# Performance work log

Hardware: AMD Instinct MI355X
Metric: run time of the kernel (lower is better)

Reference implementation:

```python
import jax, jax.numpy as jnp
import numpy as np

B = 128
DIM = 1024


def setup_inputs() -> dict:
    key = jax.random.key(0)
    k1, k2 = jax.random.split(key)
    return {
        "input1": jax.random.normal(k1, (B, DIM), dtype=jnp.float32),
        "input2": jax.random.normal(k2, (B, DIM), dtype=jnp.float32),
    }


def reference(input1, input2):
    # Original torch module computes, via a dim x dim x dim permutation tensor:
    #   cc[b, i] = sum_t input1[b, (i - t) % dim] * input2[b, t]   (circular convolution)
    # then sums over the batch and reshapes to [1, 1, dim].
    dim = input1.shape[1]
    # idx[i, t] = (i - t) mod dim  -> circulant gather of input1
    idx = (jnp.arange(dim)[:, None] - jnp.arange(dim)[None, :]) % dim
    gathered = input1[:, idx]                      # [B, dim, dim]
    cc = jnp.einsum('bit,bt->bi', gathered, input2)  # per-batch circular conv [B, dim]
    sum_rep = jnp.sum(cc, axis=0)                  # [dim]
    return sum_rep[None, None, :]                  # [1, 1, dim]
```

## Files before the change

kernel.cpp:

```cpp
#include <hip/hip_runtime.h>


#define CC_D 1024

__device__ __forceinline__ int swz(int f) {
  return (f & ~7) | ((f + (f >> 3)) & 7);
}

__global__ __launch_bounds__(512, 8) void cc_partial_kernel(
    const float* __restrict__ X, const float* __restrict__ Y,
    float* __restrict__ ws) {
  const int blk    = blockIdx.x;
  const int b      = blk >> 3;
  const int tslice = blk & 7;
  const int tid    = threadIdx.x;
  const int ig     = tid & 127;
  const int ts     = tid >> 7;

  __shared__ __align__(16) float smem[4096 + 128];
  float4* sm4 = (float4*)smem;
  float*  ysh = smem + 4096;

  if (tid < 256) {
    const float4 v = ((const float4*)(X + b * CC_D))[tid];
    sm4[swz(tid)]       = v;
    sm4[swz(tid + 256)] = v;
  }
  if (tid < 32) {
    ((float4*)ysh)[tid] =
        ((const float4*)(Y + b * CC_D + tslice * 128))[tid];
  }
  __syncthreads();

  const int ts_u = __builtin_amdgcn_readfirstlane(ts);
  const int t0   = tslice * 128 + ts_u * 32;

  const int f0 = 254 + 2 * ig - (t0 >> 2);

  float W[16];
#pragma unroll
  for (int m = 0; m < 4; ++m) {
    const float4 w = sm4[swz(f0 + m)];
    W[4 * m + 0] = w.x; W[4 * m + 1] = w.y;
    W[4 * m + 2] = w.z; W[4 * m + 3] = w.w;
  }

  float acc[8];
#pragma unroll
  for (int q = 0; q < 8; ++q) acc[q] = 0.f;

#pragma unroll
  for (int g = 0; g < 4; ++g) {
    const float4 ya = ((const float4*)ysh)[ts_u * 8 + 2 * g];
    const float4 yb = ((const float4*)ysh)[ts_u * 8 + 2 * g + 1];
    const float y[8] = {ya.x, ya.y, ya.z, ya.w, yb.x, yb.y, yb.z, yb.w};

#pragma unroll
    for (int r = 0; r < 8; ++r)
#pragma unroll
      for (int q = 0; q < 8; ++q)
        acc[q] += W[8 + q - r] * y[r];

    if (g < 3) {
#pragma unroll
      for (int j = 0; j < 8; ++j) W[8 + j] = W[j];
      const float4 w0 = sm4[swz(f0 - 2 * (g + 1))];
      const float4 w1 = sm4[swz(f0 - 2 * (g + 1) + 1)];
      W[0] = w0.x; W[1] = w0.y; W[2] = w0.z; W[3] = w0.w;
      W[4] = w1.x; W[5] = w1.y; W[6] = w1.z; W[7] = w1.w;
    }
  }

  __syncthreads();
  float4* st = (float4*)(smem + ts * CC_D + 8 * ig);
  st[0] = make_float4(acc[0], acc[1], acc[2], acc[3]);
  st[1] = make_float4(acc[4], acc[5], acc[6], acc[7]);
  __syncthreads();

  if (tid < 256) {
    float4 s = make_float4(0.f, 0.f, 0.f, 0.f);
#pragma unroll
    for (int sidx = 0; sidx < 4; ++sidx) {
      const float4 v = sm4[sidx * 256 + tid];
      s.x += v.x; s.y += v.y; s.z += v.z; s.w += v.w;
    }
    ((float4*)ws)[blk * 256 + tid] = s;
  }
}

__global__ __launch_bounds__(256) void cc_reduce_kernel(
    const float* __restrict__ ws, float* __restrict__ out) {
  const int j   = blockIdx.x;
  const int tid = threadIdx.x;

  __shared__ float4 red[256];

  float4 s = make_float4(0.f, 0.f, 0.f, 0.f);
#pragma unroll
  for (int p = 0; p < 4; ++p) {
    const float4 v = ((const float4*)ws)[(size_t)(tid + 256 * p) * 256 + j];
    s.x += v.x; s.y += v.y; s.z += v.z; s.w += v.w;
  }
  red[tid] = s;
  __syncthreads();

  for (int st = 128; st > 0; st >>= 1) {
    if (tid < st) {
      const float4 o = red[tid + st];
      red[tid].x += o.x; red[tid].y += o.y;
      red[tid].z += o.z; red[tid].w += o.w;
    }
    __syncthreads();
  }

  if (tid == 0) ((float4*)out)[j] = red[0];
}

extern "C" void kernel_launch(void* const* d_in, const int* in_sizes, int n_in,
                              void* d_out, int out_size, void* d_ws,
                              size_t ws_size, hipStream_t stream) {
  const float* X = (const float*)d_in[0];
  const float* Y = (const float*)d_in[1];
  float* out = (float*)d_out;
  float* ws  = (float*)d_ws;

  cc_partial_kernel<<<1024, 512, 0, stream>>>(X, Y, ws);
  cc_reduce_kernel<<<256, 256, 0, stream>>>(ws, out);
}
```

Baseline: 70.35 us.

## Transpose partial-sum workspace and use wave shuffles in reduction kernel

The partial kernel now reads Y directly from global memory through a wave-uniform pointer instead of staging it in shared memory. It also writes its partial sums transposed so that each reduce block reads one contiguous row. The reduce kernel replaces the shared-memory tree and its many barriers with wave-level xor shuffles followed by a four-way final sum. The partial-kernel writes become strided across blocks (each thread writes at a stride of 1024 float4s), which may hurt write coalescing in exchange for coalesced reads in the reduce.

New measurement: 64.30 us. 8.6% less time.

```diff
diff --git a/kernel.cpp b/kernel.cpp
--- a/kernel.cpp
+++ b/kernel.cpp
@@ -17,23 +17,19 @@
   const int ig     = tid & 127;
   const int ts     = tid >> 7;
 
-  __shared__ __align__(16) float smem[4096 + 128];
+  __shared__ __align__(16) float smem[4096];
   float4* sm4 = (float4*)smem;
-  float*  ysh = smem + 4096;
 
   if (tid < 256) {
     const float4 v = ((const float4*)(X + b * CC_D))[tid];
     sm4[swz(tid)]       = v;
     sm4[swz(tid + 256)] = v;
   }
-  if (tid < 32) {
-    ((float4*)ysh)[tid] =
-        ((const float4*)(Y + b * CC_D + tslice * 128))[tid];
-  }
   __syncthreads();
 
   const int ts_u = __builtin_amdgcn_readfirstlane(ts);
   const int t0   = tslice * 128 + ts_u * 32;
+  const float* yb = Y + b * CC_D + t0;
 
   const int f0 = 254 + 2 * ig - (t0 >> 2);
 
@@ -51,9 +47,9 @@
 
 #pragma unroll
   for (int g = 0; g < 4; ++g) {
-    const float4 ya = ((const float4*)ysh)[ts_u * 8 + 2 * g];
-    const float4 yb = ((const float4*)ysh)[ts_u * 8 + 2 * g + 1];
-    const float y[8] = {ya.x, ya.y, ya.z, ya.w, yb.x, yb.y, yb.z, yb.w};
+    const float4 ya = ((const float4*)(yb + 8 * g))[0];
+    const float4 yc = ((const float4*)(yb + 8 * g))[1];
+    const float y[8] = {ya.x, ya.y, ya.z, ya.w, yc.x, yc.y, yc.z, yc.w};
 
 #pragma unroll
     for (int r = 0; r < 8; ++r)
@@ -81,10 +77,10 @@
     float4 s = make_float4(0.f, 0.f, 0.f, 0.f);
 #pragma unroll
     for (int sidx = 0; sidx < 4; ++sidx) {
-      const float4 v = sm4[sidx * 256 + tid];
+      const float4 v = ((const float4*)smem)[sidx * 256 + tid];
       s.x += v.x; s.y += v.y; s.z += v.z; s.w += v.w;
     }
-    ((float4*)ws)[blk * 256 + tid] = s;
+    ((float4*)ws)[(size_t)tid * 1024 + blk] = s;
   }
 }
 
@@ -92,28 +88,36 @@
     const float* __restrict__ ws, float* __restrict__ out) {
   const int j   = blockIdx.x;
   const int tid = threadIdx.x;
+  const int l   = tid & 63;
+  const int w   = tid >> 6;
 
-  __shared__ float4 red[256];
+  __shared__ float4 red[4];
 
+  const float4* row = (const float4*)ws + (size_t)j * 1024;
   float4 s = make_float4(0.f, 0.f, 0.f, 0.f);
 #pragma unroll
-  for (int p = 0; p < 4; ++p) {
-    const float4 v = ((const float4*)ws)[(size_t)(tid + 256 * p) * 256 + j];
+  for (int c = 0; c < 4; ++c) {
+    const float4 v = row[(size_t)(c * 256 + tid)];
     s.x += v.x; s.y += v.y; s.z += v.z; s.w += v.w;
   }
-  red[tid] = s;
+#pragma unroll
+  for (int o = 32; o > 0; o >>= 1) {
+    s.x += __shfl_xor(s.x, o, 64);
+    s.y += __shfl_xor(s.y, o, 64);
+    s.z += __shfl_xor(s.z, o, 64);
+    s.w += __shfl_xor(s.w, o, 64);
+  }
+  if (l == 0) red[w] = s;
   __syncthreads();
 
-  for (int st = 128; st > 0; st >>= 1) {
-    if (tid < st) {
-      const float4 o = red[tid + st];
-      red[tid].x += o.x; red[tid].y += o.y;
-      red[tid].z += o.z; red[tid].w += o.w;
-    }
-    __syncthreads();
+  if (tid == 0) {
+    float4 r = red[0];
+    r.x += red[1].x + red[2].x + red[3].x;
+    r.y += red[1].y + red[2].y + red[3].y;
+    r.z += red[1].z + red[2].z + red[3].z;
+    r.w += red[1].w + red[2].w + red[3].w;
+    ((float4*)out)[j] = r;
   }
-
-  if (tid == 0) ((float4*)out)[j] = red[0];
 }
 
 extern "C" void kernel_launch(void* const* d_in, const int* in_sizes, int n_in,
```
